# Performance work log

Hardware: AMD Instinct MI355X
Metric: run time of the kernel (lower is better)

Reference implementation:

```python
import jax, jax.numpy as jnp
import numpy as np

N, E = 200_000, 1_000_000
WIDTH, NUM_HEAD = 128, 8
WN, WA = 1, 1            # width_norm, width_act
C = WIDTH * WN           # pre/norm channels
A = WIDTH * WA           # gate/value channels
BOND_SIZE, BAG = 33, 3
EPS = 1e-5               # GroupNorm eps (torch default)


def group_norm(x, groups, eps=EPS):
    # x: [E, C]; normalize per sample per group (affine=False, spatial size 1)
    e, c = x.shape
    xg = x.reshape(e, groups, c // groups)
    m = xg.mean(-1, keepdims=True)
    v = ((xg - m) ** 2).mean(-1, keepdims=True)
    return ((xg - m) * jax.lax.rsqrt(v + eps)).reshape(e, c)


def grouped1x1(x, w, groups):
    # grouped Conv1d with kernel 1, no bias. x: [E, Cin], w: [Cout, Cin//groups]
    e, cin = x.shape
    cout = w.shape[0]
    xg = x.reshape(e, groups, cin // groups)
    wg = w.reshape(groups, cout // groups, cin // groups)
    return jnp.einsum('egi,goi->ego', xg, wg).reshape(e, cout)


def setup_inputs() -> dict:
    key = jax.random.key(0)
    ks = jax.random.split(key, 12)
    x = jax.random.normal(ks[0], (N, WIDTH), jnp.float32)
    # degrees clamped to >= 1 in the original model
    deg = jnp.floor(jax.random.uniform(ks[1], (N,), jnp.float32, 1.0, 8.0))
    edge_idx = jax.random.randint(ks[2], (2, E), 0, N)
    edge_attr = jax.random.randint(ks[3], (E, BAG), 0, BOND_SIZE)
    s_in = 1.0 / np.sqrt(WIDTH)
    s_g = 1.0 / np.sqrt(C // NUM_HEAD)
    s_p = 1.0 / np.sqrt(A)
    pre0_w = jax.random.normal(ks[4], (C, WIDTH), jnp.float32) * s_in
    pre0_b = jnp.zeros((C,), jnp.float32)
    pre1_w = jax.random.normal(ks[5], (C, WIDTH), jnp.float32) * s_in
    pre1_b = jnp.zeros((C,), jnp.float32)
    emb = jax.random.normal(ks[6], (BOND_SIZE, C), jnp.float32)
    emb = emb.at[0].set(0.0)  # padding_idx=0
    gate_w = jax.random.normal(ks[7], (A, C // NUM_HEAD), jnp.float32) * s_g
    value_w = jax.random.normal(ks[8], (A, C // NUM_HEAD), jnp.float32) * s_g
    post_w = jax.random.normal(ks[9], (WIDTH, A), jnp.float32) * s_p
    post_b = jnp.zeros((WIDTH,), jnp.float32)
    degree_param = jnp.full((WIDTH,), -0.01, jnp.float32)
    return {"x": x, "deg": deg, "edge_idx": edge_idx, "edge_attr": edge_attr,
            "pre0_w": pre0_w, "pre0_b": pre0_b, "pre1_w": pre1_w, "pre1_b": pre1_b,
            "emb": emb, "gate_w": gate_w, "value_w": value_w,
            "post_w": post_w, "post_b": post_b, "degree_param": degree_param}


def reference(x, deg, edge_idx, edge_attr, pre0_w, pre0_b, pre1_w, pre1_b,
              emb, gate_w, value_w, post_w, post_b, degree_param):
    n = x.shape[0]
    # conv1x1 projections on nodes, then gather to edges
    h0 = x @ pre0_w.T + pre0_b                      # [N, C]
    h1 = x @ pre1_w.T + pre1_b                      # [N, C]
    xx = h0[edge_idx[0]] + h1[edge_idx[1]]          # [E, C]
    xx = group_norm(xx, NUM_HEAD)
    # EmbeddingBag mean with padding_idx=0 excluded from the mean
    mask = (edge_attr != 0)                          # [E, BAG]
    bag = (emb[edge_attr] * mask[..., None]).sum(1)  # [E, C]
    cnt = jnp.maximum(mask.sum(-1), 1).astype(xx.dtype)
    bag = bag / cnt[:, None]
    # GLU-style gate * value (Dropout is identity at eval)
    gate = jax.nn.relu(grouped1x1(xx + bag, gate_w, NUM_HEAD))  # [E, A]
    val = grouped1x1(xx, value_w, NUM_HEAD)                     # [E, A]
    xx = gate * val
    # scatter-sum back to destination nodes
    agg = jax.ops.segment_sum(xx, edge_idx[1], num_segments=n)  # [N, A]
    out = agg @ post_w.T + post_b                                # [N, WIDTH]
    out = jnp.power(deg[:, None], degree_param) * out
    return out
```

## Files before the change

kernel.cpp:

```cpp
#include <hip/hip_runtime.h>
#include <hip/hip_bf16.h>
#include <hip/hip_fp16.h>


typedef unsigned short u16;
typedef unsigned int   u32;

#define WIDTH 128

#define OFF_W0   0
#define OFF_B0   16384
#define OFF_W1   16512
#define OFF_B1   32896
#define OFF_EMB  33024
#define OFF_GW   37248
#define OFF_VW   39296
#define OFF_PW   41344
#define OFF_PB   57728
#define OFF_DP   57856
#define OFF_DEG  57984
#define ARENA_PAD 258048

typedef __attribute__((ext_vector_type(8))) short bf16x8;
typedef __attribute__((ext_vector_type(8))) _Float16 f16x8;
typedef __attribute__((ext_vector_type(4))) float f32x4;
typedef __attribute__((ext_vector_type(2))) float f32x2;
typedef __attribute__((ext_vector_type(2))) __fp16 f16x2;

__device__ __forceinline__ float b2f(u16 u){ return __uint_as_float(((u32)u) << 16); }
__device__ __forceinline__ u16   f2b(float f){
  u32 u = __float_as_uint(f);
  u += 0x7fffu + ((u >> 16) & 1u);
  return (u16)(u >> 16);
}
__device__ __forceinline__ u16   f2h(float f){ return __half_as_ushort(__float2half(f)); }
__device__ __forceinline__ float h2fl(u32 p){ return __half2float(__ushort_as_half((u16)(p & 0xffffu))); }
__device__ __forceinline__ float h2fh(u32 p){ return __half2float(__ushort_as_half((u16)(p >> 16))); }

__device__ __forceinline__ f16x2 u2h(u32 u){ union { u32 a; f16x2 b; } c; c.a = u; return c.b; }
__device__ __forceinline__ u32   h2u(f16x2 h){ union { f16x2 b; u32 a; } c; c.b = h; return c.a; }

__device__ __forceinline__ f32x2 pkfma(f32x2 a, f32x2 b, f32x2 c){
#if __has_builtin(__builtin_elementwise_fma)
  return __builtin_elementwise_fma(a, b, c);
#else
  return (f32x2){fmaf(a.x, b.x, c.x), fmaf(a.y, b.y, c.y)};
#endif
}
__device__ __forceinline__ f32x2 pkmax0(f32x2 a){
#if __has_builtin(__builtin_elementwise_max)
  return __builtin_elementwise_max(a, (f32x2){0.f, 0.f});
#else
  return (f32x2){fmaxf(a.x, 0.f), fmaxf(a.y, 0.f)};
#endif
}

#define DPPADD(s, ctrl) {                                                  \
  const float _t = __uint_as_float((u32)__builtin_amdgcn_update_dpp(       \
      0, (int)__float_as_uint(s), (ctrl), 0xF, 0xF, true));                \
  (s) += _t; }

__device__ __forceinline__ bool is_fp32(const void* degsrc){
  return ((*(const u32*)degsrc) & 0xffffu) == 0u;
}

__device__ __forceinline__ bf16x8 cvt8(float4 a, float4 b){
  bf16x8 r;
  r[0]=(short)f2b(a.x); r[1]=(short)f2b(a.y); r[2]=(short)f2b(a.z); r[3]=(short)f2b(a.w);
  r[4]=(short)f2b(b.x); r[5]=(short)f2b(b.y); r[6]=(short)f2b(b.z); r[7]=(short)f2b(b.w);
  return r;
}

__device__ __forceinline__ u16 cvt_one(const void* src, int j, bool f32){
  return f32 ? f2b(((const float*)src)[j]) : ((const u16*)src)[j];
}
__device__ __forceinline__ u16 cvt_one_h(const void* src, int j, bool f32){
  return f32 ? f2h(((const float*)src)[j]) : f2h(b2f(((const u16*)src)[j]));
}
__device__ __forceinline__ float read_f(const void* src, int j, bool f32){
  return f32 ? ((const float*)src)[j] : b2f(((const u16*)src)[j]);
}

__global__ void k_init_hist(const void* w0, const void* b0, const void* w1, const void* b1,
                            const void* emb, const void* gw, const void* vw,
                            const void* pw, const void* pb, const void* dp,
                            const void* degsrc, const int* __restrict__ eidx,
                            int* __restrict__ cnt, int E,
                            u16* __restrict__ pb16, u16* __restrict__ gembh,
                            float* __restrict__ gsums, int total)
{
  const bool f32 = is_fp32(degsrc);
  const int nbh = (E + 255) >> 8;
  const int nbc = (total + 255) >> 8;
  int b = blockIdx.x;
  const int t = threadIdx.x;

  if (b < nbh) {
    const int e = b * 256 + t;
    if (e < E) atomicAdd(&cnt[eidx[E + e]], 1);
    return;
  }
  b -= nbh;
  if (b < nbc) {
    const int i = b * 256 + t;
    if (i >= total) return;
    u16 v;
    if      (i < OFF_B0 ) v = cvt_one(w0,  i,           f32);
    else if (i < OFF_W1 ) v = cvt_one(b0,  i - OFF_B0,  f32);
    else if (i < OFF_B1 ) v = cvt_one(w1,  i - OFF_W1,  f32);
    else if (i < OFF_EMB) v = cvt_one(b1,  i - OFF_B1,  f32);
    else if (i < OFF_GW ) v = cvt_one(emb, i - OFF_EMB, f32);
    else if (i < OFF_VW ) v = cvt_one_h(gw, i - OFF_GW, f32);
    else if (i < OFF_PW ) v = cvt_one_h(vw, i - OFF_VW, f32);
    else if (i < OFF_PB ) v = cvt_one_h(pw, i - OFF_PW, f32);
    else if (i < OFF_DP ) v = cvt_one(pb,  i - OFF_PB,  f32);
    else if (i < OFF_DEG) v = cvt_one(dp,  i - OFF_DP,  f32);
    else                  v = cvt_one(degsrc, i - OFF_DEG, f32);
    pb16[i] = v;
    return;
  }
  b -= nbc;
  if (b < 17) {
    const int tid = b * 256 + t;
    if (tid >= 33 * 128) return;
    const int a = tid >> 7, c = tid & 127, g = c >> 4;
    float s = 0.f;
    #pragma unroll
    for (int i = 0; i < 16; ++i)
      s += read_f(gw, c * 16 + i, f32) * read_f(emb, a * WIDTH + g * 16 + i, f32);
    gembh[tid] = f2h(s);
    return;
  }
  if (t < 256) {
    const int c = t & 127;
    const void* src = (t >> 7) ? vw : gw;
    float s = 0.f;
    #pragma unroll
    for (int i = 0; i < 16; ++i) s += read_f(src, c * 16 + i, f32);
    gsums[t] = s;
  }
}

__global__ __launch_bounds__(256, 2) void k_pre_scan1(
    const void* __restrict__ x, const u16* __restrict__ pb16,
    u16* __restrict__ h0, u16* __restrict__ h1, const void* __restrict__ degsrc,
    const int* __restrict__ cnt, int* __restrict__ bsum, int n, int npre)
{
  if ((int)blockIdx.x >= npre) {
    const int t = threadIdx.x, b = (int)blockIdx.x - npre;
    const int i0 = b * 1024 + t * 4;
    int s = 0;
    #pragma unroll
    for (int j = 0; j < 4; ++j) { int i = i0 + j; if (i < n) s += cnt[i]; }
    __shared__ int sb[256];
    sb[t] = s; __syncthreads();
    for (int d = 128; d > 0; d >>= 1) { if (t < d) sb[t] += sb[t + d]; __syncthreads(); }
    if (t == 0) bsum[b] = sb[0];
    return;
  }

  const int t = threadIdx.x;
  const int lane = t & 63, lid = lane & 15, quad = lane >> 4;
  const int w = t >> 6, mat = w >> 1, c0 = (w & 1) * 64;
  const int node0 = blockIdx.x * 64;

  const u16* wm = pb16 + (mat ? OFF_W1 : OFF_W0);
  const u16* bs = pb16 + (mat ? OFF_B1 : OFF_B0);
  u16* hout = mat ? h1 : h0;
  const bool f32 = is_fp32(degsrc);

  f32x4 acc[4][4];
  #pragma unroll
  for (int nt = 0; nt < 4; ++nt) {
    const float bias = b2f(bs[c0 + nt * 16 + lid]);
    #pragma unroll
    for (int mt = 0; mt < 4; ++mt)
      #pragma unroll
      for (int r = 0; r < 4; ++r) acc[mt][nt][r] = bias;
  }

  #pragma unroll
  for (int ks = 0; ks < 4; ++ks) {
    bf16x8 a[4], b[4];
    #pragma unroll
    for (int nt = 0; nt < 4; ++nt)
      b[nt] = *(const bf16x8*)(wm + (size_t)(c0 + nt * 16 + lid) * WIDTH + ks * 32 + quad * 8);
    if (f32) {
      #pragma unroll
      for (int mt = 0; mt < 4; ++mt) {
        const float4* xr = (const float4*)((const float*)x +
            (size_t)(node0 + mt * 16 + lid) * WIDTH + ks * 32 + quad * 8);
        a[mt] = cvt8(xr[0], xr[1]);
      }
    } else {
      #pragma unroll
      for (int mt = 0; mt < 4; ++mt)
        a[mt] = *(const bf16x8*)((const u16*)x +
            (size_t)(node0 + mt * 16 + lid) * WIDTH + ks * 32 + quad * 8);
    }
    #pragma unroll
    for (int mt = 0; mt < 4; ++mt)
      #pragma unroll
      for (int nt = 0; nt < 4; ++nt)
        acc[mt][nt] = __builtin_amdgcn_mfma_f32_16x16x32_bf16(a[mt], b[nt], acc[mt][nt], 0, 0, 0);
  }

  #pragma unroll
  for (int mt = 0; mt < 4; ++mt)
    #pragma unroll
    for (int nt = 0; nt < 4; ++nt)
      #pragma unroll
      for (int r = 0; r < 4; ++r)
        hout[(size_t)(node0 + mt * 16 + quad * 4 + r) * WIDTH + c0 + nt * 16 + lid] =
            f2h(acc[mt][nt][r]);
}

__global__ void k_scan3(const int* __restrict__ cnt, const int* __restrict__ bsum,
                        int* __restrict__ off, int n){
  const int t = threadIdx.x, b = blockIdx.x;
  __shared__ int sp[256];
  int pv = 0;
  for (int j = t; j < b; j += 256) pv += bsum[j];
  sp[t] = pv; __syncthreads();
  for (int d = 128; d > 0; d >>= 1) { if (t < d) sp[t] += sp[t + d]; __syncthreads(); }
  const int bpref = sp[0];

  const int i0 = b * 1024 + t * 4;
  int c[4];
  #pragma unroll
  for (int j = 0; j < 4; ++j) { int i = i0 + j; c[j] = (i < n) ? cnt[i] : 0; }
  int tsum = c[0] + c[1] + c[2] + c[3];
  __shared__ int sb[256];
  sb[t] = tsum; __syncthreads();
  for (int d = 1; d < 256; d <<= 1) {
    int x = (t >= d) ? sb[t - d] : 0;
    __syncthreads();
    sb[t] += x;
    __syncthreads();
  }
  int run = bpref + sb[t] - tsum;
  #pragma unroll
  for (int j = 0; j < 4; ++j) {
    int i = i0 + j;
    if (i < n) off[i] = run;
    run += c[j];
  }
}

__global__ void k_scatter(const int* __restrict__ eidx, const int* __restrict__ eattr,
                          int* __restrict__ off, uint2* __restrict__ sedge, int E){
  const int e = blockIdx.x * 256 + threadIdx.x;
  if (e >= E) return;
  const int dst = eidx[E + e];
  const int pos = atomicAdd(&off[dst], 1);
  const u32 a0 = (u32)eattr[e*3+0], a1 = (u32)eattr[e*3+1], a2 = (u32)eattr[e*3+2];
  u32 cb = (a0 != 0) + (a1 != 0) + (a2 != 0);
  cb = cb ? cb : 1u;
  sedge[pos] = make_uint2((u32)eidx[e], a0 | (a1 << 6) | (a2 << 12) | (cb << 18));
}

__global__ __launch_bounds__(256, 4) void k_agg(
    const u16* __restrict__ h0, const u16* __restrict__ h1,
    const uint2* __restrict__ sedge, const int* __restrict__ off,
    const u16* __restrict__ pb16, const u16* __restrict__ gembh,
    const float* __restrict__ gsums, u16* __restrict__ aggh, const int N)
{
  const int base = ((blockIdx.x * 256 + threadIdx.x) >> 6) * 4;
  if (base >= N) return;
  const int q = threadIdx.x & 63;
  const int c0 = 2 * q;

  f32x2 wgl[8], wgh[8], wvl[8], wvh[8];
  {
    const u32* gp = (const u32*)(pb16 + OFF_GW + (size_t)c0 * 16);
    const u32* vp = (const u32*)(pb16 + OFF_VW + (size_t)c0 * 16);
    #pragma unroll
    for (int i = 0; i < 8; ++i) {
      const u32 ga = gp[i], gb = gp[8 + i], va = vp[i], vb = vp[8 + i];
      wgl[i] = (f32x2){h2fl(ga), h2fl(gb)};
      wgh[i] = (f32x2){h2fh(ga), h2fh(gb)};
      wvl[i] = (f32x2){h2fl(va), h2fl(vb)};
      wvh[i] = (f32x2){h2fh(va), h2fh(vb)};
    }
  }
  const f32x2 gsP = {gsums[c0], gsums[c0 + 1]};
  const f32x2 vsP = {gsums[128 + c0], gsums[128 + c0 + 1]};

  u32 h1w[4]; int nend[4];
  #pragma unroll
  for (int d = 0; d < 4; ++d) {
    const int dst = min(base + d, N - 1);
    h1w[d]  = *(const u32*)(h1 + (size_t)dst * WIDTH + c0);
    nend[d] = off[dst];
  }
  int ncur = base ? off[base - 1] : 0;
  const int nlast = nend[3];

  u32 hp = 0, g0w = 0, g1w = 0, g2w = 0; float pinv = 1.f;
  uint2 edn = make_uint2(0u, 0u);
  if (ncur < nlast) {
    const uint2 e0 = sedge[ncur];
    edn = sedge[min(ncur + 1, nlast - 1)];
    hp  = *(const u32*)(h0 + (size_t)e0.x * WIDTH + c0);
    const int a0 = e0.y & 63, a1 = (e0.y >> 6) & 63, a2 = (e0.y >> 12) & 63;
    g0w = *(const u32*)(gembh + (size_t)a0 * WIDTH + c0);
    g1w = *(const u32*)(gembh + (size_t)a1 * WIDTH + c0);
    g2w = *(const u32*)(gembh + (size_t)a2 * WIDTH + c0);
    pinv = __builtin_amdgcn_rcpf((float)((e0.y >> 18) & 3));
  }

  #pragma unroll
  for (int d = 0; d < 4; ++d) {
    const f16x2 h1h = u2h(h1w[d]);
    const int n1 = nend[d];
    f32x2 accP = (f32x2){0.f, 0.f};

    for (int i = ncur; i < n1; ++i) {
      const u32 hp_c = hp, g0c = g0w, g1c = g1w, g2c = g2w;
      const float inv_c = pinv;
      {
        const uint2 en = edn;
        edn = sedge[min(i + 2, nlast - 1)];
        hp  = *(const u32*)(h0 + (size_t)en.x * WIDTH + c0);
        const int a0 = en.y & 63, a1 = (en.y >> 6) & 63, a2 = (en.y >> 12) & 63;
        g0w = *(const u32*)(gembh + (size_t)a0 * WIDTH + c0);
        g1w = *(const u32*)(gembh + (size_t)a1 * WIDTH + c0);
        g2w = *(const u32*)(gembh + (size_t)a2 * WIDTH + c0);
        pinv = __builtin_amdgcn_rcpf((float)((en.y >> 18) & 3));
      }

      const f16x2 xh = u2h(hp_c) + h1h;
      const u32 xu = h2u(xh);
      const float x0f = (float)xh.x, x1f = (float)xh.y;

      float s  = x0f + x1f;
      float ss = fmaf(x0f, x0f, x1f * x1f);
      DPPADD(s, 0xB1);  DPPADD(ss, 0xB1);
      DPPADD(s, 0x4E);  DPPADD(ss, 0x4E);
      DPPADD(s, 0x141); DPPADD(ss, 0x141);
      const float mean = s * 0.0625f;
      const float var  = fmaf(ss, 0.0625f, -mean * mean);
      const float rs   = __builtin_amdgcn_rsqf(var + 1e-5f);
      const float mrs  = mean * rs;

      f32x2 gaP = (f32x2){0.f, 0.f}, vaP = (f32x2){0.f, 0.f};
#define CSTEP(J) {                                                             \
      const u32 xj = (u32)__builtin_amdgcn_ds_swizzle((int)xu, 0x18 | ((J) << 5)); \
      const float xl = h2fl(xj), xhv = h2fh(xj);                               \
      const f32x2 xlP = {xl, xl}, xhP = {xhv, xhv};                            \
      gaP = pkfma(xlP, wgl[J], gaP); gaP = pkfma(xhP, wgh[J], gaP);            \
      vaP = pkfma(xlP, wvl[J], vaP); vaP = pkfma(xhP, wvh[J], vaP); }
      CSTEP(0) CSTEP(1) CSTEP(2) CSTEP(3) CSTEP(4) CSTEP(5) CSTEP(6) CSTEP(7)
#undef CSTEP

      const f16x2 gsum3 = u2h(g0c) + u2h(g1c) + u2h(g2c);
      const f32x2 invP  = {inv_c, inv_c};
      const f32x2 bgP   = (f32x2){(float)gsum3.x, (float)gsum3.y} * invP;

      const f32x2 rsP = {rs, rs}, nmP = {-mrs, -mrs};
      const f32x2 gate = pkfma(rsP, gaP, pkfma(nmP, gsP, bgP));
      const f32x2 val  = pkfma(rsP, vaP, nmP * vsP);
      accP = pkfma(pkmax0(gate), val, accP);
    }

    if (base + d < N)
      *(u32*)(aggh + (size_t)(base + d) * WIDTH + c0) =
          h2u(__builtin_amdgcn_cvt_pkrtz(accP.x, accP.y));
    ncur = n1;
  }
}

__global__ __launch_bounds__(256, 2) void k_post(
    const u16* __restrict__ aggh, const u16* __restrict__ pb16,
    void* __restrict__ out, const void* __restrict__ degsrc)
{
  const int t = threadIdx.x;
  const int lane = t & 63, lid = lane & 15, quad = lane >> 4;
  const int w = t >> 6, c0 = (w & 1) * 64, mh = (w >> 1) * 32;
  const int node0 = blockIdx.x * 64;
  const bool f32o = is_fp32(degsrc);

  f32x4 acc[2][4];
  float dpc[4];
  #pragma unroll
  for (int nt = 0; nt < 4; ++nt) {
    const float bias = b2f(pb16[OFF_PB + c0 + nt * 16 + lid]);
    dpc[nt] = b2f(pb16[OFF_DP + c0 + nt * 16 + lid]);
    #pragma unroll
    for (int mt = 0; mt < 2; ++mt)
      #pragma unroll
      for (int r = 0; r < 4; ++r) acc[mt][nt][r] = bias;
  }

  #pragma unroll
  for (int ks = 0; ks < 4; ++ks) {
    f16x8 a[2], b[4];
    #pragma unroll
    for (int nt = 0; nt < 4; ++nt)
      b[nt] = *(const f16x8*)(pb16 + OFF_PW + (size_t)(c0 + nt * 16 + lid) * WIDTH + ks * 32 + quad * 8);
    #pragma unroll
    for (int mt = 0; mt < 2; ++mt)
      a[mt] = *(const f16x8*)(aggh +
          (size_t)(node0 + mh + mt * 16 + lid) * WIDTH + ks * 32 + quad * 8);
    #pragma unroll
    for (int mt = 0; mt < 2; ++mt)
      #pragma unroll
      for (int nt = 0; nt < 4; ++nt)
        acc[mt][nt] = __builtin_amdgcn_mfma_f32_16x16x32_f16(a[mt], b[nt], acc[mt][nt], 0, 0, 0);
  }

  float logd[2][4];
  #pragma unroll
  for (int mt = 0; mt < 2; ++mt)
    #pragma unroll
    for (int r = 0; r < 4; ++r)
      logd[mt][r] = __logf(b2f(pb16[OFF_DEG + node0 + mh + mt * 16 + quad * 4 + r]));

  #pragma unroll
  for (int mt = 0; mt < 2; ++mt)
    #pragma unroll
    for (int nt = 0; nt < 4; ++nt)
      #pragma unroll
      for (int r = 0; r < 4; ++r) {
        const int node = node0 + mh + mt * 16 + quad * 4 + r;
        const float v = acc[mt][nt][r] * __expf(dpc[nt] * logd[mt][r]);
        if (f32o) ((float*)out)[(size_t)node * WIDTH + c0 + nt * 16 + lid] = v;
        else      ((u16*)out)[(size_t)node * WIDTH + c0 + nt * 16 + lid] = f2b(v);
      }
}

extern "C" void kernel_launch(void* const* d_in, const int* in_sizes, int n_in,
                              void* d_out, int out_size, void* d_ws, size_t ws_size,
                              hipStream_t stream)
{
  (void)n_in; (void)out_size; (void)ws_size;
  const void* x     = d_in[0];
  const void* deg   = d_in[1];
  const int*  eidx  = (const int*)d_in[2];
  const int*  eattr = (const int*)d_in[3];

  const int N = in_sizes[1];
  const int E = in_sizes[2] / 2;

  u16*   aggh = (u16*)d_ws;
  u16*   h1   = (u16*)((float*)d_ws + (size_t)N * WIDTH);
  u16*   pb16 = h1 + (size_t)N * WIDTH;
  u16*   gembh= pb16 + ARENA_PAD;
  float* gsums= (float*)(gembh + 33 * WIDTH);
  int*   cnt  = (int*)(gsums + 256);
  int*   off  = cnt + N;
  int*   bsum = off + N;
  uint2* sedge= (uint2*)(bsum + 1024);
  u16*   h0   = (u16*)d_out;

  const int total = OFF_DEG + N;
  const int nbc = (total + 255) / 256;
  const int nbh = (E + 255) / 256;

  hipMemsetAsync(cnt, 0, (size_t)N * sizeof(int), stream);

  k_init_hist<<<nbh + nbc + 18, 256, 0, stream>>>(
      d_in[4], d_in[5], d_in[6], d_in[7], d_in[8], d_in[9], d_in[10],
      d_in[11], d_in[12], d_in[13], deg, eidx, cnt, E, pb16, gembh, gsums, total);

  const int npre = N / 64;
  const int nblk = (N + 1023) / 1024;
  k_pre_scan1<<<npre + nblk, 256, 0, stream>>>(
      x, pb16, h0, h1, deg, cnt, bsum, N, npre);

  k_scan3  <<<nblk, 256, 0, stream>>>(cnt, bsum, off, N);
  k_scatter<<<nbh, 256, 0, stream>>>(eidx, eattr, off, sedge, E);

  k_agg<<<((size_t)N * 16 + 255) / 256, 256, 0, stream>>>(
      h0, h1, sedge, off, pb16, gembh, gsums, aggh, N);

  k_post<<<N / 64, 256, 0, stream>>>(aggh, pb16, d_out, deg);
}
```

Measured before the change: 630.3 us.

## Precompute per-node gate/value projections of h0 and move the rest into the loop

```diff
diff --git a/kernel.cpp b/kernel.cpp
--- a/kernel.cpp
+++ b/kernel.cpp
@@ -18,13 +18,16 @@
 #define OFF_PW   41344
 #define OFF_PB   57728
 #define OFF_DP   57856
-#define OFF_DEG  57984
-#define ARENA_PAD 258048
+#define OFF_WGC  57984
+#define OFF_WVC  74368
+#define OFF_BGC  90752
+#define OFF_BVC  90880
+#define OFF_DEG  91008
+#define ARENA_PAD 291072
 
 typedef __attribute__((ext_vector_type(8))) short bf16x8;
 typedef __attribute__((ext_vector_type(8))) _Float16 f16x8;
 typedef __attribute__((ext_vector_type(4))) float f32x4;
-typedef __attribute__((ext_vector_type(2))) float f32x2;
 typedef __attribute__((ext_vector_type(2))) __fp16 f16x2;
 
 __device__ __forceinline__ float b2f(u16 u){ return __uint_as_float(((u32)u) << 16); }
@@ -34,24 +37,16 @@
   return (u16)(u >> 16);
 }
 __device__ __forceinline__ u16   f2h(float f){ return __half_as_ushort(__float2half(f)); }
-__device__ __forceinline__ float h2fl(u32 p){ return __half2float(__ushort_as_half((u16)(p & 0xffffu))); }
-__device__ __forceinline__ float h2fh(u32 p){ return __half2float(__ushort_as_half((u16)(p >> 16))); }
+__device__ __forceinline__ float h2f(u16 u){ return __half2float(__ushort_as_half(u)); }
 
 __device__ __forceinline__ f16x2 u2h(u32 u){ union { u32 a; f16x2 b; } c; c.a = u; return c.b; }
 __device__ __forceinline__ u32   h2u(f16x2 h){ union { f16x2 b; u32 a; } c; c.b = h; return c.a; }
 
-__device__ __forceinline__ f32x2 pkfma(f32x2 a, f32x2 b, f32x2 c){
+__device__ __forceinline__ f16x2 pkhfma(f16x2 a, f16x2 b, f16x2 c){
 #if __has_builtin(__builtin_elementwise_fma)
   return __builtin_elementwise_fma(a, b, c);
 #else
-  return (f32x2){fmaf(a.x, b.x, c.x), fmaf(a.y, b.y, c.y)};
-#endif
-}
-__device__ __forceinline__ f32x2 pkmax0(f32x2 a){
-#if __has_builtin(__builtin_elementwise_max)
-  return __builtin_elementwise_max(a, (f32x2){0.f, 0.f});
-#else
-  return (f32x2){fmaxf(a.x, 0.f), fmaxf(a.y, 0.f)};
+  return a * b + c;
 #endif
 }
 
@@ -68,6 +63,18 @@
   bf16x8 r;
   r[0]=(short)f2b(a.x); r[1]=(short)f2b(a.y); r[2]=(short)f2b(a.z); r[3]=(short)f2b(a.w);
   r[4]=(short)f2b(b.x); r[5]=(short)f2b(b.y); r[6]=(short)f2b(b.z); r[7]=(short)f2b(b.w);
+  return r;
+}
+__device__ __forceinline__ f16x8 cvt8h(float4 a, float4 b){
+  f16x8 r;
+  r[0]=(_Float16)a.x; r[1]=(_Float16)a.y; r[2]=(_Float16)a.z; r[3]=(_Float16)a.w;
+  r[4]=(_Float16)b.x; r[5]=(_Float16)b.y; r[6]=(_Float16)b.z; r[7]=(_Float16)b.w;
+  return r;
+}
+__device__ __forceinline__ f16x8 cvtbh(bf16x8 v){
+  f16x8 r;
+  #pragma unroll
+  for (int j = 0; j < 8; ++j) r[j] = (_Float16)b2f((u16)v[j]);
   return r;
 }
 
@@ -87,11 +94,12 @@
                             const void* degsrc, const int* __restrict__ eidx,
                             int* __restrict__ cnt, int E,
                             u16* __restrict__ pb16, u16* __restrict__ gembh,
-                            float* __restrict__ gsums, int total)
+                            float* __restrict__ gsums, int N)
 {
   const bool f32 = is_fp32(degsrc);
   const int nbh = (E + 255) >> 8;
-  const int nbc = (total + 255) >> 8;
+  const int tot_cvt = OFF_WGC + N;
+  const int nbc = (tot_cvt + 255) >> 8;
   int b = blockIdx.x;
   const int t = threadIdx.x;
 
@@ -103,8 +111,8 @@
   b -= nbh;
   if (b < nbc) {
     const int i = b * 256 + t;
-    if (i >= total) return;
-    u16 v;
+    if (i >= tot_cvt) return;
+    u16 v; int dsti = i;
     if      (i < OFF_B0 ) v = cvt_one(w0,  i,           f32);
     else if (i < OFF_W1 ) v = cvt_one(b0,  i - OFF_B0,  f32);
     else if (i < OFF_B1 ) v = cvt_one(w1,  i - OFF_W1,  f32);
@@ -114,9 +122,9 @@
     else if (i < OFF_PW ) v = cvt_one_h(vw, i - OFF_VW, f32);
     else if (i < OFF_PB ) v = cvt_one_h(pw, i - OFF_PW, f32);
     else if (i < OFF_DP ) v = cvt_one(pb,  i - OFF_PB,  f32);
-    else if (i < OFF_DEG) v = cvt_one(dp,  i - OFF_DP,  f32);
-    else                  v = cvt_one(degsrc, i - OFF_DEG, f32);
-    pb16[i] = v;
+    else if (i < OFF_WGC) v = cvt_one(dp,  i - OFF_DP,  f32);
+    else { v = cvt_one(degsrc, i - OFF_WGC, f32); dsti = OFF_DEG + (i - OFF_WGC); }
+    pb16[dsti] = v;
     return;
   }
   b -= nbc;
@@ -131,30 +139,60 @@
     gembh[tid] = f2h(s);
     return;
   }
+  b -= 17;
+  if (b < 1) {
+    if (t < 256) {
+      const int c = t & 127;
+      const void* src = (t >> 7) ? vw : gw;
+      float s = 0.f;
+      #pragma unroll
+      for (int i = 0; i < 16; ++i) s += read_f(src, c * 16 + i, f32);
+      gsums[t] = s;
+    }
+    return;
+  }
+  b -= 1;
+  if (b < 128) {
+    const int tid = b * 256 + t;
+    const int m = tid >> 14;
+    const int o = (tid >> 7) & 127;
+    const int i = tid & 127;
+    const void* wsel = m ? vw : gw;
+    const int hb = (o >> 4) * 16;
+    float s = 0.f;
+    #pragma unroll
+    for (int j = 0; j < 16; ++j)
+      s += read_f(wsel, o * 16 + j, f32) * read_f(w0, (size_t)(hb + j) * 128 + i, f32);
+    pb16[(m ? OFF_WVC : OFF_WGC) + o * 128 + i] = f2h(s);
+    return;
+  }
   if (t < 256) {
-    const int c = t & 127;
-    const void* src = (t >> 7) ? vw : gw;
+    const int m = t >> 7, o = t & 127, hb = (o >> 4) * 16;
+    const void* wsel = m ? vw : gw;
     float s = 0.f;
     #pragma unroll
-    for (int i = 0; i < 16; ++i) s += read_f(src, c * 16 + i, f32);
-    gsums[t] = s;
-  }
-}
-
-__global__ __launch_bounds__(256, 2) void k_pre_scan1(
+    for (int j = 0; j < 16; ++j)
+      s += read_f(wsel, o * 16 + j, f32) * read_f(b0, hb + j, f32);
+    pb16[(m ? OFF_BVC : OFF_BGC) + o] = f2h(s);
+  }
+}
+
+__global__ __launch_bounds__(512, 2) void k_pre_scan1(
     const void* __restrict__ x, const u16* __restrict__ pb16,
-    u16* __restrict__ h0, u16* __restrict__ h1, const void* __restrict__ degsrc,
+    u16* __restrict__ h0, u16* __restrict__ h1,
+    u16* __restrict__ ug0, u16* __restrict__ uv0,
+    const void* __restrict__ degsrc,
     const int* __restrict__ cnt, int* __restrict__ bsum, int n, int npre)
 {
   if ((int)blockIdx.x >= npre) {
     const int t = threadIdx.x, b = (int)blockIdx.x - npre;
-    const int i0 = b * 1024 + t * 4;
+    const int i0 = b * 1024 + t * 2;
     int s = 0;
-    #pragma unroll
-    for (int j = 0; j < 4; ++j) { int i = i0 + j; if (i < n) s += cnt[i]; }
-    __shared__ int sb[256];
+    if (i0     < n) s += cnt[i0];
+    if (i0 + 1 < n) s += cnt[i0 + 1];
+    __shared__ int sb[512];
     sb[t] = s; __syncthreads();
-    for (int d = 128; d > 0; d >>= 1) { if (t < d) sb[t] += sb[t + d]; __syncthreads(); }
+    for (int d = 256; d > 0; d >>= 1) { if (t < d) sb[t] += sb[t + d]; __syncthreads(); }
     if (t == 0) bsum[b] = sb[0];
     return;
   }
@@ -163,55 +201,86 @@
   const int lane = t & 63, lid = lane & 15, quad = lane >> 4;
   const int w = t >> 6, mat = w >> 1, c0 = (w & 1) * 64;
   const int node0 = blockIdx.x * 64;
-
-  const u16* wm = pb16 + (mat ? OFF_W1 : OFF_W0);
-  const u16* bs = pb16 + (mat ? OFF_B1 : OFF_B0);
-  u16* hout = mat ? h1 : h0;
   const bool f32 = is_fp32(degsrc);
 
+  const u16* wsrc; const u16* bsv; u16* dstp;
+  if      (mat == 0) { wsrc = pb16 + OFF_W0;  bsv = pb16 + OFF_B0;  dstp = h0;  }
+  else if (mat == 1) { wsrc = pb16 + OFF_W1;  bsv = pb16 + OFF_B1;  dstp = h1;  }
+  else if (mat == 2) { wsrc = pb16 + OFF_WGC; bsv = pb16 + OFF_BGC; dstp = ug0; }
+  else               { wsrc = pb16 + OFF_WVC; bsv = pb16 + OFF_BVC; dstp = uv0; }
+
   f32x4 acc[4][4];
   #pragma unroll
   for (int nt = 0; nt < 4; ++nt) {
-    const float bias = b2f(bs[c0 + nt * 16 + lid]);
+    const u16 braw = bsv[c0 + nt * 16 + lid];
+    const float bias = (mat < 2) ? b2f(braw) : h2f(braw);
     #pragma unroll
     for (int mt = 0; mt < 4; ++mt)
       #pragma unroll
       for (int r = 0; r < 4; ++r) acc[mt][nt][r] = bias;
   }
 
-  #pragma unroll
-  for (int ks = 0; ks < 4; ++ks) {
-    bf16x8 a[4], b[4];
+  if (mat < 2) {
+    #pragma unroll
+    for (int ks = 0; ks < 4; ++ks) {
+      bf16x8 a[4], b[4];
+      #pragma unroll
+      for (int nt = 0; nt < 4; ++nt)
+        b[nt] = *(const bf16x8*)(wsrc + (size_t)(c0 + nt * 16 + lid) * WIDTH + ks * 32 + quad * 8);
+      if (f32) {
+        #pragma unroll
+        for (int mt = 0; mt < 4; ++mt) {
+          const float4* xr = (const float4*)((const float*)x +
+              (size_t)(node0 + mt * 16 + lid) * WIDTH + ks * 32 + quad * 8);
+          a[mt] = cvt8(xr[0], xr[1]);
+        }
+      } else {
+        #pragma unroll
+        for (int mt = 0; mt < 4; ++mt)
+          a[mt] = *(const bf16x8*)((const u16*)x +
+              (size_t)(node0 + mt * 16 + lid) * WIDTH + ks * 32 + quad * 8);
+      }
+      #pragma unroll
+      for (int mt = 0; mt < 4; ++mt)
+        #pragma unroll
+        for (int nt = 0; nt < 4; ++nt)
+          acc[mt][nt] = __builtin_amdgcn_mfma_f32_16x16x32_bf16(a[mt], b[nt], acc[mt][nt], 0, 0, 0);
+    }
+  } else {
+    #pragma unroll
+    for (int ks = 0; ks < 4; ++ks) {
+      f16x8 a[4], b[4];
+      #pragma unroll
+      for (int nt = 0; nt < 4; ++nt)
+        b[nt] = *(const f16x8*)(wsrc + (size_t)(c0 + nt * 16 + lid) * WIDTH + ks * 32 + quad * 8);
+      if (f32) {
+        #pragma unroll
+        for (int mt = 0; mt < 4; ++mt) {
+          const float4* xr = (const float4*)((const float*)x +
+              (size_t)(node0 + mt * 16 + lid) * WIDTH + ks * 32 + quad * 8);
+          a[mt] = cvt8h(xr[0], xr[1]);
+        }
+      } else {
+        #pragma unroll
+        for (int mt = 0; mt < 4; ++mt)
+          a[mt] = cvtbh(*(const bf16x8*)((const u16*)x +
+              (size_t)(node0 + mt * 16 + lid) * WIDTH + ks * 32 + quad * 8));
+      }
+      #pragma unroll
+      for (int mt = 0; mt < 4; ++mt)
+        #pragma unroll
+        for (int nt = 0; nt < 4; ++nt)
+          acc[mt][nt] = __builtin_amdgcn_mfma_f32_16x16x32_f16(a[mt], b[nt], acc[mt][nt], 0, 0, 0);
+    }
+  }
+
+  #pragma unroll
+  for (int mt = 0; mt < 4; ++mt)
     #pragma unroll
     for (int nt = 0; nt < 4; ++nt)
-      b[nt] = *(const bf16x8*)(wm + (size_t)(c0 + nt * 16 + lid) * WIDTH + ks * 32 + quad * 8);
-    if (f32) {
-      #pragma unroll
-      for (int mt = 0; mt < 4; ++mt) {
-        const float4* xr = (const float4*)((const float*)x +
-            (size_t)(node0 + mt * 16 + lid) * WIDTH + ks * 32 + quad * 8);
-        a[mt] = cvt8(xr[0], xr[1]);
-      }
-    } else {
-      #pragma unroll
-      for (int mt = 0; mt < 4; ++mt)
-        a[mt] = *(const bf16x8*)((const u16*)x +
-            (size_t)(node0 + mt * 16 + lid) * WIDTH + ks * 32 + quad * 8);
-    }
-    #pragma unroll
-    for (int mt = 0; mt < 4; ++mt)
-      #pragma unroll
-      for (int nt = 0; nt < 4; ++nt)
-        acc[mt][nt] = __builtin_amdgcn_mfma_f32_16x16x32_bf16(a[mt], b[nt], acc[mt][nt], 0, 0, 0);
-  }
-
-  #pragma unroll
-  for (int mt = 0; mt < 4; ++mt)
-    #pragma unroll
-    for (int nt = 0; nt < 4; ++nt)
       #pragma unroll
       for (int r = 0; r < 4; ++r)
-        hout[(size_t)(node0 + mt * 16 + quad * 4 + r) * WIDTH + c0 + nt * 16 + lid] =
+        dstp[(size_t)(node0 + mt * 16 + quad * 4 + r) * WIDTH + c0 + nt * 16 + lid] =
             f2h(acc[mt][nt][r]);
 }
 
@@ -261,6 +330,7 @@
 
 __global__ __launch_bounds__(256, 4) void k_agg(
     const u16* __restrict__ h0, const u16* __restrict__ h1,
+    const u16* __restrict__ ug0, const u16* __restrict__ uv0,
     const uint2* __restrict__ sedge, const int* __restrict__ off,
     const u16* __restrict__ pb16, const u16* __restrict__ gembh,
     const float* __restrict__ gsums, u16* __restrict__ aggh, const int N)
@@ -270,21 +340,18 @@
   const int q = threadIdx.x & 63;
   const int c0 = 2 * q;
 
-  f32x2 wgl[8], wgh[8], wvl[8], wvh[8];
+  u32 gw0[8], gw1[8], vw0[8], vw1[8];
   {
-    const u32* gp = (const u32*)(pb16 + OFF_GW + (size_t)c0 * 16);
-    const u32* vp = (const u32*)(pb16 + OFF_VW + (size_t)c0 * 16);
+    const u32* g = (const u32*)(pb16 + OFF_GW + (size_t)c0 * 16);
+    const u32* v = (const u32*)(pb16 + OFF_VW + (size_t)c0 * 16);
     #pragma unroll
     for (int i = 0; i < 8; ++i) {
-      const u32 ga = gp[i], gb = gp[8 + i], va = vp[i], vb = vp[8 + i];
-      wgl[i] = (f32x2){h2fl(ga), h2fl(gb)};
-      wgh[i] = (f32x2){h2fh(ga), h2fh(gb)};
-      wvl[i] = (f32x2){h2fl(va), h2fl(vb)};
-      wvh[i] = (f32x2){h2fh(va), h2fh(vb)};
+      gw0[i] = g[i]; gw1[i] = g[8 + i];
+      vw0[i] = v[i]; vw1[i] = v[8 + i];
     }
   }
-  const f32x2 gsP = {gsums[c0], gsums[c0 + 1]};
-  const f32x2 vsP = {gsums[128 + c0], gsums[128 + c0 + 1]};
+  const float gs0 = gsums[c0],       gs1 = gsums[c0 + 1];
+  const float vs0 = gsums[128 + c0], vs1 = gsums[128 + c0 + 1];
 
   u32 h1w[4]; int nend[4];
   #pragma unroll
@@ -296,12 +363,15 @@
   int ncur = base ? off[base - 1] : 0;
   const int nlast = nend[3];
 
-  u32 hp = 0, g0w = 0, g1w = 0, g2w = 0; float pinv = 1.f;
+  u32 hp = 0, ugp = 0, uvp = 0, g0w = 0, g1w = 0, g2w = 0; float pinv = 1.f;
   uint2 edn = make_uint2(0u, 0u);
   if (ncur < nlast) {
     const uint2 e0 = sedge[ncur];
     edn = sedge[min(ncur + 1, nlast - 1)];
-    hp  = *(const u32*)(h0 + (size_t)e0.x * WIDTH + c0);
+    const size_t vo = (size_t)e0.x * WIDTH + c0;
+    hp  = *(const u32*)(h0  + vo);
+    ugp = *(const u32*)(ug0 + vo);
+    uvp = *(const u32*)(uv0 + vo);
     const int a0 = e0.y & 63, a1 = (e0.y >> 6) & 63, a2 = (e0.y >> 12) & 63;
     g0w = *(const u32*)(gembh + (size_t)a0 * WIDTH + c0);
     g1w = *(const u32*)(gembh + (size_t)a1 * WIDTH + c0);
@@ -312,16 +382,36 @@
   #pragma unroll
   for (int d = 0; d < 4; ++d) {
     const f16x2 h1h = u2h(h1w[d]);
+
+    f16x2 ag0 = u2h(0), ag1 = u2h(0), av0 = u2h(0), av1 = u2h(0);
+#define DSTEP(J) {                                                             \
+    const f16x2 xj = u2h((u32)__builtin_amdgcn_ds_swizzle(                     \
+        (int)h1w[d], 0x18 | ((J) << 5)));                                      \
+    ag0 = pkhfma(xj, u2h(gw0[J]), ag0);                                        \
+    ag1 = pkhfma(xj, u2h(gw1[J]), ag1);                                        \
+    av0 = pkhfma(xj, u2h(vw0[J]), av0);                                        \
+    av1 = pkhfma(xj, u2h(vw1[J]), av1); }
+    DSTEP(0) DSTEP(1) DSTEP(2) DSTEP(3) DSTEP(4) DSTEP(5) DSTEP(6) DSTEP(7)
+#undef DSTEP
+    const float ug1d0 = (float)ag0.x + (float)ag0.y;
+    const float ug1d1 = (float)ag1.x + (float)ag1.y;
+    const float uv1d0 = (float)av0.x + (float)av0.y;
+    const float uv1d1 = (float)av1.x + (float)av1.y;
+
     const int n1 = nend[d];
-    f32x2 accP = (f32x2){0.f, 0.f};
+    float acc0 = 0.f, acc1 = 0.f;
 
     for (int i = ncur; i < n1; ++i) {
-      const u32 hp_c = hp, g0c = g0w, g1c = g1w, g2c = g2w;
+      const u32 hp_c = hp, ug_c = ugp, uv_c = uvp;
+      const u32 g0c = g0w, g1c = g1w, g2c = g2w;
       const float inv_c = pinv;
       {
         const uint2 en = edn;
         edn = sedge[min(i + 2, nlast - 1)];
-        hp  = *(const u32*)(h0 + (size_t)en.x * WIDTH + c0);
+        const size_t vo = (size_t)en.x * WIDTH + c0;
+        hp  = *(const u32*)(h0  + vo);
+        ugp = *(const u32*)(ug0 + vo);
+        uvp = *(const u32*)(uv0 + vo);
         const int a0 = en.y & 63, a1 = (en.y >> 6) & 63, a2 = (en.y >> 12) & 63;
         g0w = *(const u32*)(gembh + (size_t)a0 * WIDTH + c0);
         g1w = *(const u32*)(gembh + (size_t)a1 * WIDTH + c0);
@@ -330,11 +420,10 @@
       }
 
       const f16x2 xh = u2h(hp_c) + h1h;
-      const u32 xu = h2u(xh);
-      const float x0f = (float)xh.x, x1f = (float)xh.y;
-
-      float s  = x0f + x1f;
-      float ss = fmaf(x0f, x0f, x1f * x1f);
+      const float x0 = (float)xh.x, x1 = (float)xh.y;
+
+      float s  = x0 + x1;
+      float ss = fmaf(x0, x0, x1 * x1);
       DPPADD(s, 0xB1);  DPPADD(ss, 0xB1);
       DPPADD(s, 0x4E);  DPPADD(ss, 0x4E);
       DPPADD(s, 0x141); DPPADD(ss, 0x141);
@@ -343,29 +432,22 @@
       const float rs   = __builtin_amdgcn_rsqf(var + 1e-5f);
       const float mrs  = mean * rs;
 
-      f32x2 gaP = (f32x2){0.f, 0.f}, vaP = (f32x2){0.f, 0.f};
-#define CSTEP(J) {                                                             \
-      const u32 xj = (u32)__builtin_amdgcn_ds_swizzle((int)xu, 0x18 | ((J) << 5)); \
-      const float xl = h2fl(xj), xhv = h2fh(xj);                               \
-      const f32x2 xlP = {xl, xl}, xhP = {xhv, xhv};                            \
-      gaP = pkfma(xlP, wgl[J], gaP); gaP = pkfma(xhP, wgh[J], gaP);            \
-      vaP = pkfma(xlP, wvl[J], vaP); vaP = pkfma(xhP, wvh[J], vaP); }
-      CSTEP(0) CSTEP(1) CSTEP(2) CSTEP(3) CSTEP(4) CSTEP(5) CSTEP(6) CSTEP(7)
-#undef CSTEP
-
-      const f16x2 gsum3 = u2h(g0c) + u2h(g1c) + u2h(g2c);
-      const f32x2 invP  = {inv_c, inv_c};
-      const f32x2 bgP   = (f32x2){(float)gsum3.x, (float)gsum3.y} * invP;
-
-      const f32x2 rsP = {rs, rs}, nmP = {-mrs, -mrs};
-      const f32x2 gate = pkfma(rsP, gaP, pkfma(nmP, gsP, bgP));
-      const f32x2 val  = pkfma(rsP, vaP, nmP * vsP);
-      accP = pkfma(pkmax0(gate), val, accP);
+      const f16x2 bsum3 = u2h(g0c) + u2h(g1c) + u2h(g2c);
+      const float bg0 = (float)bsum3.x * inv_c;
+      const float bg1 = (float)bsum3.y * inv_c;
+
+      const f16x2 ugh = u2h(ug_c), uvh = u2h(uv_c);
+      const float gate0 = fmaf(rs, (float)ugh.x + ug1d0, fmaf(-mrs, gs0, bg0));
+      const float gate1 = fmaf(rs, (float)ugh.y + ug1d1, fmaf(-mrs, gs1, bg1));
+      const float val0  = fmaf(rs, (float)uvh.x + uv1d0, -mrs * vs0);
+      const float val1  = fmaf(rs, (float)uvh.y + uv1d1, -mrs * vs1);
+      acc0 = fmaf(fmaxf(gate0, 0.f), val0, acc0);
+      acc1 = fmaf(fmaxf(gate1, 0.f), val1, acc1);
     }
 
     if (base + d < N)
       *(u32*)(aggh + (size_t)(base + d) * WIDTH + c0) =
-          h2u(__builtin_amdgcn_cvt_pkrtz(accP.x, accP.y));
+          h2u(__builtin_amdgcn_cvt_pkrtz(acc0, acc1));
     ncur = n1;
   }
 }
@@ -443,8 +525,10 @@
   const int E = in_sizes[2] / 2;
 
   u16*   aggh = (u16*)d_ws;
-  u16*   h1   = (u16*)((float*)d_ws + (size_t)N * WIDTH);
-  u16*   pb16 = h1 + (size_t)N * WIDTH;
+  u16*   h1   = aggh + (size_t)N * WIDTH;
+  u16*   ug0  = h1   + (size_t)N * WIDTH;
+  u16*   uv0  = ug0  + (size_t)N * WIDTH;
+  u16*   pb16 = uv0  + (size_t)N * WIDTH;
   u16*   gembh= pb16 + ARENA_PAD;
   float* gsums= (float*)(gembh + 33 * WIDTH);
   int*   cnt  = (int*)(gsums + 256);
@@ -453,26 +537,25 @@
   uint2* sedge= (uint2*)(bsum + 1024);
   u16*   h0   = (u16*)d_out;
 
-  const int total = OFF_DEG + N;
-  const int nbc = (total + 255) / 256;
+  const int nbc = (OFF_WGC + N + 255) / 256;
   const int nbh = (E + 255) / 256;
 
   hipMemsetAsync(cnt, 0, (size_t)N * sizeof(int), stream);
 
-  k_init_hist<<<nbh + nbc + 18, 256, 0, stream>>>(
+  k_init_hist<<<nbh + nbc + 17 + 1 + 128 + 1, 256, 0, stream>>>(
       d_in[4], d_in[5], d_in[6], d_in[7], d_in[8], d_in[9], d_in[10],
-      d_in[11], d_in[12], d_in[13], deg, eidx, cnt, E, pb16, gembh, gsums, total);
+      d_in[11], d_in[12], d_in[13], deg, eidx, cnt, E, pb16, gembh, gsums, N);
 
   const int npre = N / 64;
   const int nblk = (N + 1023) / 1024;
-  k_pre_scan1<<<npre + nblk, 256, 0, stream>>>(
-      x, pb16, h0, h1, deg, cnt, bsum, N, npre);
+  k_pre_scan1<<<npre + nblk, 512, 0, stream>>>(
+      x, pb16, h0, h1, ug0, uv0, deg, cnt, bsum, N, npre);
 
   k_scan3  <<<nblk, 256, 0, stream>>>(cnt, bsum, off, N);
   k_scatter<<<nbh, 256, 0, stream>>>(eidx, eattr, off, sedge, E);
 
   k_agg<<<((size_t)N * 16 + 255) / 256, 256, 0, stream>>>(
-      h0, h1, sedge, off, pb16, gembh, gsums, aggh, N);
+      h0, h1, ug0, uv0, sedge, off, pb16, gembh, gsums, aggh, N);
 
   k_post<<<N / 64, 256, 0, stream>>>(aggh, pb16, d_out, deg);
 }
```

After: 679.8 us. 7.9% more time.
